# Kernel optimization log

Measured on AMD Instinct MI355X. Metric: run time of the kernel, lower is better.

## Reference

```python
import jax, jax.numpy as jnp
import numpy as np

N, D = 8192, 1024
TEMPERATURE = 0.1
EPS = 1e-8

def setup_inputs() -> dict:
    key = jax.random.key(0)
    k1, k2 = jax.random.split(key)
    emb = jax.random.normal(k1, (N, D), dtype=jnp.float32)
    # docstring: embeddings are normalized
    emb = emb / jnp.linalg.norm(emb, axis=1, keepdims=True)
    labels = jax.random.randint(k2, (N,), 0, 2, dtype=jnp.int32)
    return {"embeddings": emb, "labels": labels}

def reference(embeddings, labels):
    lab = labels.astype(embeddings.dtype)            # (N,)
    sim = jnp.matmul(embeddings, embeddings.T) / TEMPERATURE  # (N, N)
    exp_sim = jnp.exp(sim)                           # original uses raw exp (no max-subtract)
    diag = jnp.diagonal(exp_sim)                     # self-similarity exp(1/T)
    # all_sim excludes self; pos_sim = other reference rows (labels==1, j != i)
    all_sum = exp_sim.sum(axis=1) - diag             # (N,)
    pos_sum = exp_sim @ lab - diag * lab             # subtract self only when i is ref
    loss_per_row = -jnp.log(pos_sum / (all_sum + EPS))
    n_ref = lab.sum()
    loss = jnp.sum(jnp.where(lab > 0, loss_per_row, 0.0)) / jnp.maximum(n_ref, 1.0)
    # original returns 0.0 when fewer than 2 reference rows
    return jnp.where(n_ref < 2, jnp.array(0.0, embeddings.dtype), loss)
```

## Files before the change

kernel.cpp:

```cpp
#include <hip/hip_runtime.h>
#include <hip/hip_bf16.h>
#include <cstdint>
#include <cstddef>

#define NROWS 8192
#define DIM   1024
#define BM 128
#define BN 128
#define BK 64
#define EPS 1e-8f
#define PRESCALE 3.798288f

typedef short  bf16x8  __attribute__((ext_vector_type(8)));
typedef float  floatx4 __attribute__((ext_vector_type(4)));

typedef __attribute__((address_space(1))) const void CGV;
typedef __attribute__((address_space(3))) void LV;

__device__ __forceinline__ void async_load16(const void* g, void* l) {
    __builtin_amdgcn_global_load_lds((CGV*)g, (LV*)l, 16, 0, 0);
}

__device__ __forceinline__ unsigned short f2bf_rne(float f) {
    union { float f; unsigned u; } c; c.f = f;
    unsigned u = c.u;
    unsigned r = (u + 0x7fffu + ((u >> 16) & 1u)) >> 16;
    return (unsigned short)r;
}

__global__ __launch_bounds__(256) void convert_kernel(
    const float* __restrict__ in, unsigned short* __restrict__ out,
    float* __restrict__ accum )
{
    int i = (blockIdx.x * 256 + threadIdx.x) * 4;
    float4 v = *(const float4*)(in + i);
    ushort4 o;
    o.x = f2bf_rne(v.x * PRESCALE);
    o.y = f2bf_rne(v.y * PRESCALE);
    o.z = f2bf_rne(v.z * PRESCALE);
    o.w = f2bf_rne(v.w * PRESCALE);
    *(ushort4*)(out + i) = o;
    if (blockIdx.x < (2 * NROWS) / 256)
        accum[blockIdx.x * 256 + threadIdx.x] = 0.0f;
}

__global__ __launch_bounds__(256, 4) void gemm_fused_kernel(
    const unsigned short* __restrict__ E,
    const int*            __restrict__ labels,
    float*                __restrict__ all_sum,
    float*                __restrict__ pos_sum)
{
    __shared__ __align__(16) unsigned short sA[BM * BK];
    __shared__ __align__(16) unsigned short sB[BN * BK];

    const int tid  = threadIdx.x;
    const int lane = tid & 63;
    const int w    = tid >> 6;
    const int wm   = w >> 1;
    const int wn   = w & 1;
    const int colw = lane & 15;
    const int quad = lane >> 4;

    const int b = blockIdx.x;
    const int t = (b & 7) * 260 + (b >> 3);
    int bi = (int)((sqrtf(8.0f * (float)t + 1.0f) - 1.0f) * 0.5f);
    while ((bi + 1) * (bi + 2) / 2 <= t) ++bi;
    while (bi * (bi + 1) / 2 > t) --bi;
    const int bj = t - bi * (bi + 1) / 2;

    const int rBase = bi * BM;
    const int cBase = bj * BN;
    const bool diag = (bi == bj);

    const int srow = tid >> 3;
    const int scol = (((tid & 7) ^ (srow & 7)) << 3);
    const int e0   = tid * 8;

    floatx4 acc[4][4];
    #pragma unroll
    for (int i = 0; i < 4; ++i)
        #pragma unroll
        for (int j = 0; j < 4; ++j)
            acc[i][j] = (floatx4)0.0f;

    const int swz   = colw & 7;
    const int aRow0 = (wm * 64 + colw) * BK;
    const int bRow0 = (wn * 64 + colw) * BK;

    const size_t gA0 = (size_t)(rBase + srow) * DIM + scol;
    const size_t gB0 = (size_t)(cBase + srow) * DIM + scol;
    const size_t rstep = (size_t)32 * DIM;

    for (int k0 = 0; k0 < DIM; k0 += BK) {
        __syncthreads();
        async_load16(E + gA0 + k0,             &sA[e0]);
        async_load16(E + gA0 + rstep + k0,     &sA[e0 + 2048]);
        async_load16(E + gA0 + 2 * rstep + k0, &sA[e0 + 4096]);
        async_load16(E + gA0 + 3 * rstep + k0, &sA[e0 + 6144]);
        async_load16(E + gB0 + k0,             &sB[e0]);
        async_load16(E + gB0 + rstep + k0,     &sB[e0 + 2048]);
        async_load16(E + gB0 + 2 * rstep + k0, &sB[e0 + 4096]);
        async_load16(E + gB0 + 3 * rstep + k0, &sB[e0 + 6144]);
        __syncthreads();

        #pragma unroll
        for (int h = 0; h < 2; ++h) {
            const int cOff = (((h << 2) | quad) ^ swz) << 3;
            bf16x8 aF[4], bF[4];
            #pragma unroll
            for (int mt = 0; mt < 4; ++mt)
                aF[mt] = *(const bf16x8*)&sA[aRow0 + mt * 16 * BK + cOff];
            #pragma unroll
            for (int nt = 0; nt < 4; ++nt)
                bF[nt] = *(const bf16x8*)&sB[bRow0 + nt * 16 * BK + cOff];

            #pragma unroll
            for (int mt = 0; mt < 4; ++mt)
                #pragma unroll
                for (int nt = 0; nt < 4; ++nt)
                    acc[mt][nt] = __builtin_amdgcn_mfma_f32_16x16x32_bf16(
                        aF[mt], bF[nt], acc[mt][nt], 0, 0, 0);
        }
    }

    float labc[4];
    int   gcol[4];
    #pragma unroll
    for (int nt = 0; nt < 4; ++nt) {
        gcol[nt] = cBase + wn * 64 + nt * 16 + colw;
        labc[nt] = (float)labels[gcol[nt]];
    }

    float colAll[4] = {0.f, 0.f, 0.f, 0.f};
    float colPos[4] = {0.f, 0.f, 0.f, 0.f};

    #pragma unroll
    for (int mt = 0; mt < 4; ++mt) {
        const int growBase = rBase + wm * 64 + mt * 16 + quad * 4;
        #pragma unroll
        for (int r = 0; r < 4; ++r) {
            const int grow = growBase + r;
            const float labr = (float)labels[grow];
            float sAll = 0.f, sPos = 0.f;
            #pragma unroll
            for (int nt = 0; nt < 4; ++nt) {
                float ev = exp2f(acc[mt][nt][r]);
                if (diag && grow == gcol[nt]) ev = 0.0f;
                sAll += ev;
                sPos += ev * labc[nt];
                colAll[nt] += ev;
                colPos[nt] += ev * labr;
            }
            #pragma unroll
            for (int off = 1; off < 16; off <<= 1) {
                sAll += __shfl_xor(sAll, off);
                sPos += __shfl_xor(sPos, off);
            }
            if (colw == 0) {
                atomicAdd(&all_sum[grow], sAll);
                atomicAdd(&pos_sum[grow], sPos);
            }
        }
    }

    if (!diag) {
        #pragma unroll
        for (int nt = 0; nt < 4; ++nt) {
            float a = colAll[nt], p = colPos[nt];
            a += __shfl_xor(a, 16);  p += __shfl_xor(p, 16);
            a += __shfl_xor(a, 32);  p += __shfl_xor(p, 32);
            if (quad == 0) {
                atomicAdd(&all_sum[gcol[nt]], a);
                atomicAdd(&pos_sum[gcol[nt]], p);
            }
        }
    }
}

__global__ __launch_bounds__(1024) void finalize_kernel(
    const float* __restrict__ all_sum,
    const float* __restrict__ pos_sum,
    const int*   __restrict__ labels,
    float*       __restrict__ out)
{
    __shared__ float sSum[1024];
    __shared__ float sCnt[1024];
    const int tid = threadIdx.x;
    float lsum = 0.f, lcnt = 0.f;
    for (int i = tid; i < NROWS; i += 1024) {
        if (labels[i] > 0) {
            float p = pos_sum[i];
            float a = all_sum[i] + EPS;
            lsum += -logf(p / a);
            lcnt += 1.0f;
        }
    }
    sSum[tid] = lsum;
    sCnt[tid] = lcnt;
    __syncthreads();
    for (int s = 512; s > 0; s >>= 1) {
        if (tid < s) { sSum[tid] += sSum[tid + s]; sCnt[tid] += sCnt[tid + s]; }
        __syncthreads();
    }
    if (tid == 0) {
        float n = sCnt[0];
        out[0] = (n < 2.0f) ? 0.0f : sSum[0] / fmaxf(n, 1.0f);
    }
}

extern "C" void kernel_launch(void* const* d_in, const int* in_sizes, int n_in,
                              void* d_out, int out_size, void* d_ws, size_t ws_size,
                              hipStream_t stream) {
    const float* emb    = (const float*)d_in[0];
    const int*   labels = (const int*)d_in[1];
    float*       out    = (float*)d_out;

    unsigned short* Ebf = (unsigned short*)d_ws;
    const size_t embBytes = (size_t)NROWS * DIM * sizeof(unsigned short);
    float* all_sum = (float*)((char*)d_ws + embBytes);
    float* pos_sum = all_sum + NROWS;

    convert_kernel<<<(NROWS * DIM) / (4 * 256), 256, 0, stream>>>(emb, Ebf, all_sum);

    const int nBlocksTri = (NROWS / BM) * (NROWS / BM + 1) / 2;
    gemm_fused_kernel<<<nBlocksTri, 256, 0, stream>>>(Ebf, labels, all_sum, pos_sum);

    finalize_kernel<<<1, 1024, 0, stream>>>(all_sum, pos_sum, labels, out);
}
```

Before: 210.5 us.

## Switch similarity GEMM from bf16 to fp8 with scaled MFMA 16x16x128

Converts the prescaled embeddings to fp8 (e4m3) instead of bf16 and computes the Gram matrix with the MI355X scaled f8f6f4 MFMA at K=128 per instruction. The K tile, LDS layout, swizzle and fragment loads are reworked for byte-sized elements, and occupancy hint drops to 3. This halves the operand bytes and raises matrix throughput per instruction. The cost is much lower precision in a similarity that is then exponentiated at temperature 0.1, so loss accuracy may suffer.

```diff
diff --git a/kernel.cpp b/kernel.cpp
--- a/kernel.cpp
+++ b/kernel.cpp
@@ -7,11 +7,11 @@
 #define DIM   1024
 #define BM 128
 #define BN 128
-#define BK 64
+#define BKB 128
 #define EPS 1e-8f
 #define PRESCALE 3.798288f
 
-typedef short  bf16x8  __attribute__((ext_vector_type(8)));
+typedef int    intx8   __attribute__((ext_vector_type(8)));
 typedef float  floatx4 __attribute__((ext_vector_type(4)));
 
 typedef __attribute__((address_space(1))) const void CGV;
@@ -21,37 +21,36 @@
     __builtin_amdgcn_global_load_lds((CGV*)g, (LV*)l, 16, 0, 0);
 }
 
-__device__ __forceinline__ unsigned short f2bf_rne(float f) {
-    union { float f; unsigned u; } c; c.f = f;
-    unsigned u = c.u;
-    unsigned r = (u + 0x7fffu + ((u >> 16) & 1u)) >> 16;
-    return (unsigned short)r;
+__device__ __forceinline__ intx8 ldfrag(const unsigned char* base, int o0, int o1) {
+    int4 lo = *(const int4*)(base + o0);
+    int4 hi = *(const int4*)(base + o1);
+    intx8 r;
+    r[0] = lo.x; r[1] = lo.y; r[2] = lo.z; r[3] = lo.w;
+    r[4] = hi.x; r[5] = hi.y; r[6] = hi.z; r[7] = hi.w;
+    return r;
 }
 
 __global__ __launch_bounds__(256) void convert_kernel(
-    const float* __restrict__ in, unsigned short* __restrict__ out,
+    const float* __restrict__ in, unsigned int* __restrict__ out,
     float* __restrict__ accum )
 {
     int i = (blockIdx.x * 256 + threadIdx.x) * 4;
     float4 v = *(const float4*)(in + i);
-    ushort4 o;
-    o.x = f2bf_rne(v.x * PRESCALE);
-    o.y = f2bf_rne(v.y * PRESCALE);
-    o.z = f2bf_rne(v.z * PRESCALE);
-    o.w = f2bf_rne(v.w * PRESCALE);
-    *(ushort4*)(out + i) = o;
+    int p = __builtin_amdgcn_cvt_pk_fp8_f32(v.x * PRESCALE, v.y * PRESCALE, 0, false);
+    p     = __builtin_amdgcn_cvt_pk_fp8_f32(v.z * PRESCALE, v.w * PRESCALE, p, true);
+    out[i >> 2] = (unsigned int)p;
     if (blockIdx.x < (2 * NROWS) / 256)
         accum[blockIdx.x * 256 + threadIdx.x] = 0.0f;
 }
 
-__global__ __launch_bounds__(256, 4) void gemm_fused_kernel(
-    const unsigned short* __restrict__ E,
-    const int*            __restrict__ labels,
-    float*                __restrict__ all_sum,
-    float*                __restrict__ pos_sum)
+__global__ __launch_bounds__(256, 3) void gemm_fused_kernel(
+    const unsigned char* __restrict__ E,
+    const int*           __restrict__ labels,
+    float*               __restrict__ all_sum,
+    float*               __restrict__ pos_sum)
 {
-    __shared__ __align__(16) unsigned short sA[BM * BK];
-    __shared__ __align__(16) unsigned short sB[BN * BK];
+    __shared__ __align__(16) unsigned char sA[BM * BKB];
+    __shared__ __align__(16) unsigned char sB[BN * BKB];
 
     const int tid  = threadIdx.x;
     const int lane = tid & 63;
@@ -73,8 +72,8 @@
     const bool diag = (bi == bj);
 
     const int srow = tid >> 3;
-    const int scol = (((tid & 7) ^ (srow & 7)) << 3);
-    const int e0   = tid * 8;
+    const int scol = (((tid & 7) ^ (srow & 7)) << 4);
+    const int e0   = tid * 16;
 
     floatx4 acc[4][4];
     #pragma unroll
@@ -83,43 +82,43 @@
         for (int j = 0; j < 4; ++j)
             acc[i][j] = (floatx4)0.0f;
 
-    const int swz   = colw & 7;
-    const int aRow0 = (wm * 64 + colw) * BK;
-    const int bRow0 = (wn * 64 + colw) * BK;
+    const int swz  = colw & 7;
+    const int c0   = (((quad << 1)    ) ^ swz) << 4;
+    const int c1   = (((quad << 1) | 1) ^ swz) << 4;
+    const int aRow0 = (wm * 64 + colw) * BKB;
+    const int bRow0 = (wn * 64 + colw) * BKB;
 
     const size_t gA0 = (size_t)(rBase + srow) * DIM + scol;
     const size_t gB0 = (size_t)(cBase + srow) * DIM + scol;
     const size_t rstep = (size_t)32 * DIM;
 
-    for (int k0 = 0; k0 < DIM; k0 += BK) {
+    for (int k0 = 0; k0 < DIM; k0 += BKB) {
         __syncthreads();
         async_load16(E + gA0 + k0,             &sA[e0]);
-        async_load16(E + gA0 + rstep + k0,     &sA[e0 + 2048]);
-        async_load16(E + gA0 + 2 * rstep + k0, &sA[e0 + 4096]);
-        async_load16(E + gA0 + 3 * rstep + k0, &sA[e0 + 6144]);
+        async_load16(E + gA0 + rstep + k0,     &sA[e0 + 4096]);
+        async_load16(E + gA0 + 2 * rstep + k0, &sA[e0 + 8192]);
+        async_load16(E + gA0 + 3 * rstep + k0, &sA[e0 + 12288]);
         async_load16(E + gB0 + k0,             &sB[e0]);
-        async_load16(E + gB0 + rstep + k0,     &sB[e0 + 2048]);
-        async_load16(E + gB0 + 2 * rstep + k0, &sB[e0 + 4096]);
-        async_load16(E + gB0 + 3 * rstep + k0, &sB[e0 + 6144]);
+        async_load16(E + gB0 + rstep + k0,     &sB[e0 + 4096]);
+        async_load16(E + gB0 + 2 * rstep + k0, &sB[e0 + 8192]);
+        async_load16(E + gB0 + 3 * rstep + k0, &sB[e0 + 12288]);
         __syncthreads();
 
-        #pragma unroll
-        for (int h = 0; h < 2; ++h) {
-            const int cOff = (((h << 2) | quad) ^ swz) << 3;
-            bf16x8 aF[4], bF[4];
+        intx8 aF[4];
+        #pragma unroll
+        for (int mt = 0; mt < 4; ++mt)
+            aF[mt] = ldfrag(&sA[aRow0 + mt * 16 * BKB], c0, c1);
+
+        #pragma unroll
+        for (int nt = 0; nt < 4; ++nt) {
+            intx8 bF = ldfrag(&sB[bRow0 + nt * 16 * BKB], c0, c1);
             #pragma unroll
             for (int mt = 0; mt < 4; ++mt)
-                aF[mt] = *(const bf16x8*)&sA[aRow0 + mt * 16 * BK + cOff];
-            #pragma unroll
-            for (int nt = 0; nt < 4; ++nt)
-                bF[nt] = *(const bf16x8*)&sB[bRow0 + nt * 16 * BK + cOff];
-
-            #pragma unroll
-            for (int mt = 0; mt < 4; ++mt)
-                #pragma unroll
-                for (int nt = 0; nt < 4; ++nt)
-                    acc[mt][nt] = __builtin_amdgcn_mfma_f32_16x16x32_bf16(
-                        aF[mt], bF[nt], acc[mt][nt], 0, 0, 0);
+                acc[mt][nt] = __builtin_amdgcn_mfma_scale_f32_16x16x128_f8f6f4(
+                    aF[mt], bF, acc[mt][nt],
+                    0, 0,
+                    0, 127,
+                    0, 127);
         }
     }
 
@@ -215,15 +214,16 @@
     const int*   labels = (const int*)d_in[1];
     float*       out    = (float*)d_out;
 
-    unsigned short* Ebf = (unsigned short*)d_ws;
-    const size_t embBytes = (size_t)NROWS * DIM * sizeof(unsigned short);
+    unsigned char* Efp8 = (unsigned char*)d_ws;
+    const size_t embBytes = (size_t)NROWS * DIM;
     float* all_sum = (float*)((char*)d_ws + embBytes);
     float* pos_sum = all_sum + NROWS;
 
-    convert_kernel<<<(NROWS * DIM) / (4 * 256), 256, 0, stream>>>(emb, Ebf, all_sum);
+    convert_kernel<<<(NROWS * DIM) / (4 * 256), 256, 0, stream>>>(
+        emb, (unsigned int*)Efp8, all_sum);
 
     const int nBlocksTri = (NROWS / BM) * (NROWS / BM + 1) / 2;
-    gemm_fused_kernel<<<nBlocksTri, 256, 0, stream>>>(Ebf, labels, all_sum, pos_sum);
+    gemm_fused_kernel<<<nBlocksTri, 256, 0, stream>>>(Efp8, labels, all_sum, pos_sum);
 
     finalize_kernel<<<1, 1024, 0, stream>>>(all_sum, pos_sum, labels, out);
 }
```

Result: slower. 547.1 us (+160.0%).

## Use 256x128 rectangular tiles over lower triangle with strict-lower masking

Applied to the files above, without the earlier changes.

Replaces the 128x128 triangular tile enumeration with 256x128 tiles covering the lower triangle (I rows of 256, J up to 2I+1 column tiles), giving each wave a 64x128 output strip for more MFMA work per LDS load. The diagonal is handled by masking every element with grow > gcol, so each off-diagonal pair is counted once through the row and column scatters. Warps whose rows lie entirely above the diagonal skip the epilogue, and zero-valued atomics are skipped. Occupancy drops to 2 blocks per CU and accumulator register use doubles, and some upper-triangle MFMA work is still computed and then discarded.

```diff
diff --git a/kernel.cpp b/kernel.cpp
--- a/kernel.cpp
+++ b/kernel.cpp
@@ -5,9 +5,10 @@
 
 #define NROWS 8192
 #define DIM   1024
-#define BM 128
-#define BN 128
-#define BK 64
+#define BMR 256
+#define BNC 128
+#define BK  64
+#define NBLK 1056
 #define EPS 1e-8f
 #define PRESCALE 3.798288f
 
@@ -44,48 +45,45 @@
         accum[blockIdx.x * 256 + threadIdx.x] = 0.0f;
 }
 
-__global__ __launch_bounds__(256, 4) void gemm_fused_kernel(
+__global__ __launch_bounds__(256, 2) void gemm_fused_kernel(
     const unsigned short* __restrict__ E,
     const int*            __restrict__ labels,
     float*                __restrict__ all_sum,
     float*                __restrict__ pos_sum)
 {
-    __shared__ __align__(16) unsigned short sA[BM * BK];
-    __shared__ __align__(16) unsigned short sB[BN * BK];
+    __shared__ __align__(16) unsigned short sA[BMR * BK];
+    __shared__ __align__(16) unsigned short sB[BNC * BK];
 
     const int tid  = threadIdx.x;
     const int lane = tid & 63;
     const int w    = tid >> 6;
-    const int wm   = w >> 1;
-    const int wn   = w & 1;
     const int colw = lane & 15;
     const int quad = lane >> 4;
 
     const int b = blockIdx.x;
-    const int t = (b & 7) * 260 + (b >> 3);
-    int bi = (int)((sqrtf(8.0f * (float)t + 1.0f) - 1.0f) * 0.5f);
-    while ((bi + 1) * (bi + 2) / 2 <= t) ++bi;
-    while (bi * (bi + 1) / 2 > t) --bi;
-    const int bj = t - bi * (bi + 1) / 2;
-
-    const int rBase = bi * BM;
-    const int cBase = bj * BN;
-    const bool diag = (bi == bj);
+    const int t = (b & 7) * 132 + (b >> 3);
+    int I = (int)((sqrtf(4.0f * (float)t + 1.0f) - 1.0f) * 0.5f);
+    while ((I + 1) * (I + 2) <= t) ++I;
+    while (I * (I + 1) > t) --I;
+    const int J = t - I * (I + 1);
+
+    const int rBase = I * BMR;
+    const int cBase = J * BNC;
 
     const int srow = tid >> 3;
     const int scol = (((tid & 7) ^ (srow & 7)) << 3);
     const int e0   = tid * 8;
 
-    floatx4 acc[4][4];
+    floatx4 acc[4][8];
     #pragma unroll
     for (int i = 0; i < 4; ++i)
         #pragma unroll
-        for (int j = 0; j < 4; ++j)
+        for (int j = 0; j < 8; ++j)
             acc[i][j] = (floatx4)0.0f;
 
     const int swz   = colw & 7;
-    const int aRow0 = (wm * 64 + colw) * BK;
-    const int bRow0 = (wn * 64 + colw) * BK;
+    const int aRow0 = (w * 64 + colw) * BK;
+    const int bRow0 = colw * BK;
 
     const size_t gA0 = (size_t)(rBase + srow) * DIM + scol;
     const size_t gB0 = (size_t)(cBase + srow) * DIM + scol;
@@ -93,59 +91,59 @@
 
     for (int k0 = 0; k0 < DIM; k0 += BK) {
         __syncthreads();
-        async_load16(E + gA0 + k0,             &sA[e0]);
-        async_load16(E + gA0 + rstep + k0,     &sA[e0 + 2048]);
-        async_load16(E + gA0 + 2 * rstep + k0, &sA[e0 + 4096]);
-        async_load16(E + gA0 + 3 * rstep + k0, &sA[e0 + 6144]);
-        async_load16(E + gB0 + k0,             &sB[e0]);
-        async_load16(E + gB0 + rstep + k0,     &sB[e0 + 2048]);
-        async_load16(E + gB0 + 2 * rstep + k0, &sB[e0 + 4096]);
-        async_load16(E + gB0 + 3 * rstep + k0, &sB[e0 + 6144]);
+        #pragma unroll
+        for (int j = 0; j < 8; ++j)
+            async_load16(E + gA0 + j * rstep + k0, &sA[e0 + j * 2048]);
+        #pragma unroll
+        for (int j = 0; j < 4; ++j)
+            async_load16(E + gB0 + j * rstep + k0, &sB[e0 + j * 2048]);
         __syncthreads();
 
         #pragma unroll
         for (int h = 0; h < 2; ++h) {
             const int cOff = (((h << 2) | quad) ^ swz) << 3;
-            bf16x8 aF[4], bF[4];
+            bf16x8 aF[4], bF[8];
             #pragma unroll
             for (int mt = 0; mt < 4; ++mt)
                 aF[mt] = *(const bf16x8*)&sA[aRow0 + mt * 16 * BK + cOff];
             #pragma unroll
-            for (int nt = 0; nt < 4; ++nt)
+            for (int nt = 0; nt < 8; ++nt)
                 bF[nt] = *(const bf16x8*)&sB[bRow0 + nt * 16 * BK + cOff];
 
             #pragma unroll
             for (int mt = 0; mt < 4; ++mt)
                 #pragma unroll
-                for (int nt = 0; nt < 4; ++nt)
+                for (int nt = 0; nt < 8; ++nt)
                     acc[mt][nt] = __builtin_amdgcn_mfma_f32_16x16x32_bf16(
                         aF[mt], bF[nt], acc[mt][nt], 0, 0, 0);
         }
     }
 
-    float labc[4];
-    int   gcol[4];
-    #pragma unroll
-    for (int nt = 0; nt < 4; ++nt) {
-        gcol[nt] = cBase + wn * 64 + nt * 16 + colw;
+    if (rBase + w * 64 + 63 < cBase) return;
+
+    float labc[8];
+    int   gcol[8];
+    #pragma unroll
+    for (int nt = 0; nt < 8; ++nt) {
+        gcol[nt] = cBase + nt * 16 + colw;
         labc[nt] = (float)labels[gcol[nt]];
     }
 
-    float colAll[4] = {0.f, 0.f, 0.f, 0.f};
-    float colPos[4] = {0.f, 0.f, 0.f, 0.f};
+    float colAll[8] = {0.f, 0.f, 0.f, 0.f, 0.f, 0.f, 0.f, 0.f};
+    float colPos[8] = {0.f, 0.f, 0.f, 0.f, 0.f, 0.f, 0.f, 0.f};
 
     #pragma unroll
     for (int mt = 0; mt < 4; ++mt) {
-        const int growBase = rBase + wm * 64 + mt * 16 + quad * 4;
+        const int growBase = rBase + w * 64 + mt * 16 + quad * 4;
         #pragma unroll
         for (int r = 0; r < 4; ++r) {
             const int grow = growBase + r;
             const float labr = (float)labels[grow];
             float sAll = 0.f, sPos = 0.f;
             #pragma unroll
-            for (int nt = 0; nt < 4; ++nt) {
+            for (int nt = 0; nt < 8; ++nt) {
                 float ev = exp2f(acc[mt][nt][r]);
-                if (diag && grow == gcol[nt]) ev = 0.0f;
+                ev = (grow > gcol[nt]) ? ev : 0.0f;
                 sAll += ev;
                 sPos += ev * labc[nt];
                 colAll[nt] += ev;
@@ -156,23 +154,21 @@
                 sAll += __shfl_xor(sAll, off);
                 sPos += __shfl_xor(sPos, off);
             }
-            if (colw == 0) {
+            if (colw == 0 && sAll != 0.f) {
                 atomicAdd(&all_sum[grow], sAll);
                 atomicAdd(&pos_sum[grow], sPos);
             }
         }
     }
 
-    if (!diag) {
-        #pragma unroll
-        for (int nt = 0; nt < 4; ++nt) {
-            float a = colAll[nt], p = colPos[nt];
-            a += __shfl_xor(a, 16);  p += __shfl_xor(p, 16);
-            a += __shfl_xor(a, 32);  p += __shfl_xor(p, 32);
-            if (quad == 0) {
-                atomicAdd(&all_sum[gcol[nt]], a);
-                atomicAdd(&pos_sum[gcol[nt]], p);
-            }
+    #pragma unroll
+    for (int nt = 0; nt < 8; ++nt) {
+        float a = colAll[nt], p = colPos[nt];
+        a += __shfl_xor(a, 16);  p += __shfl_xor(p, 16);
+        a += __shfl_xor(a, 32);  p += __shfl_xor(p, 32);
+        if (quad == 0 && a != 0.f) {
+            atomicAdd(&all_sum[gcol[nt]], a);
+            atomicAdd(&pos_sum[gcol[nt]], p);
         }
     }
 }
@@ -222,8 +218,7 @@
 
     convert_kernel<<<(NROWS * DIM) / (4 * 256), 256, 0, stream>>>(emb, Ebf, all_sum);
 
-    const int nBlocksTri = (NROWS / BM) * (NROWS / BM + 1) / 2;
-    gemm_fused_kernel<<<nBlocksTri, 256, 0, stream>>>(Ebf, labels, all_sum, pos_sum);
+    gemm_fused_kernel<<<NBLK, 256, 0, stream>>>(Ebf, labels, all_sum, pos_sum);
 
     finalize_kernel<<<1, 1024, 0, stream>>>(all_sum, pos_sum, labels, out);
 }
```

Result: faster. 186.0 us (-11.6%).
